# Performance work log

Measured on AMD Instinct MI355X. Metric: run time of the kernel, lower is better.

The kernel has to match this reference:

```python
import jax, jax.numpy as jnp
import numpy as np

B, T, C = 4, 4096, 512
H, KS = 8, 9
D = C // H
PAD = KS // 2


def setup_inputs() -> dict:
    key = jax.random.key(0)
    ks = jax.random.split(key, 9)
    s = 1.0 / np.sqrt(C)
    return {
        "x": jax.random.normal(ks[0], (B, T, C), jnp.float32),
        "Wq": jax.random.normal(ks[1], (C, C), jnp.float32) * s,
        "bq": jax.random.normal(ks[2], (C,), jnp.float32) * 0.01,
        "Wk": jax.random.normal(ks[3], (C, C), jnp.float32) * s,
        "bk": jax.random.normal(ks[4], (C,), jnp.float32) * 0.01,
        "Wv": jax.random.normal(ks[5], (C, C), jnp.float32) * s,
        "bv": jax.random.normal(ks[6], (C,), jnp.float32) * 0.01,
        "Wo": jax.random.normal(ks[7], (C, C), jnp.float32) * s,
        "bo": jax.random.normal(ks[8], (C,), jnp.float32) * 0.01,
    }


def reference(x, Wq, bq, Wk, bk, Wv, bv, Wo, bo):
    Bx, Tx, Cx = x.shape
    # projections (torch Linear: x @ W.T + b), split heads -> (B,H,T,D)
    q = (x @ Wq.T + bq).reshape(Bx, Tx, H, D).transpose(0, 2, 1, 3)
    k = (x @ Wk.T + bk).reshape(Bx, Tx, H, D).transpose(0, 2, 1, 3)
    v = (x @ Wv.T + bv).reshape(Bx, Tx, H, D).transpose(0, 2, 1, 3)
    # replicate-pad along time (matches F.pad mode='replicate')
    k_pad = jnp.pad(k, ((0, 0), (0, 0), (PAD, PAD), (0, 0)), mode='edge')
    v_pad = jnp.pad(v, ((0, 0), (0, 0), (PAD, PAD), (0, 0)), mode='edge')
    # window gather indices: (T, KS) into padded time axis
    idx = jnp.arange(Tx)[:, None] + jnp.arange(KS)[None, :]
    k_unf = k_pad[:, :, idx, :]  # (B,H,T,KS,D)
    v_unf = v_pad[:, :, idx, :]  # (B,H,T,KS,D)
    scale = 1.0 / np.sqrt(D)
    scores = jnp.einsum('bhtd,bhtkd->bhtk', q, k_unf) * scale  # (B,H,T,KS)
    attn = jax.nn.softmax(scores, axis=-1)
    y = jnp.einsum('bhtk,bhtkd->bhtd', attn, v_unf)  # (B,H,T,D)
    y = y.transpose(0, 2, 1, 3).reshape(Bx, Tx, Cx)
    return y @ Wo.T + bo
```

## Files before the change

kernel.cpp:

```cpp
#include <hip/hip_runtime.h>
#include <hip/hip_bf16.h>

#define B_    4
#define T_    4096
#define C_    512
#define H_    8
#define D_    64
#define KS_   9
#define PAD_  4
#define MTOT  (B_ * T_)
#define PLANE (MTOT * C_)
#define XU    (MTOT * C_ / 8)
#define WU    (C_ * C_ / 8)

typedef __bf16 bf16_t;
typedef __bf16 bf16x8 __attribute__((ext_vector_type(8)));
typedef float  f32x4  __attribute__((ext_vector_type(4)));

__global__ __launch_bounds__(256)
void conv_all(const float* __restrict__ x,  const float* __restrict__ Wq,
              const float* __restrict__ Wk, const float* __restrict__ Wv,
              const float* __restrict__ Wo, bf16_t* __restrict__ dst) {
  int i = blockIdx.x * 256 + threadIdx.x;
  const float* s;
  if (i < XU) {
    s = x + (size_t)i * 8;
  } else {
    int r = i - XU;
    int w = r >> 15;
    const float* W = (w == 0) ? Wq : (w == 1) ? Wk : (w == 2) ? Wv : Wo;
    s = W + (size_t)(r & (WU - 1)) * 8;
  }
  float4 f0 = ((const float4*)s)[0];
  float4 f1 = ((const float4*)s)[1];
  bf16x8 o;
  o[0] = (bf16_t)f0.x; o[1] = (bf16_t)f0.y; o[2] = (bf16_t)f0.z; o[3] = (bf16_t)f0.w;
  o[4] = (bf16_t)f1.x; o[5] = (bf16_t)f1.y; o[6] = (bf16_t)f1.z; o[7] = (bf16_t)f1.w;
  ((bf16x8*)dst)[i] = o;
}

__global__ __launch_bounds__(256, 2)
void qkv_gemm(const bf16_t* __restrict__ xb, const bf16_t* __restrict__ Wb,
              const float* __restrict__ bq, const float* __restrict__ bk,
              const float* __restrict__ bv, bf16_t* __restrict__ qkv) {
  __shared__ __align__(16) bf16_t lsA[256 * 64];
  __shared__ __align__(16) bf16_t lsB[128 * 64];

  const int z    = blockIdx.z;
  const int m0   = blockIdx.y * 256;
  const int n0   = blockIdx.x * 128;
  const bf16_t* W = Wb + (size_t)z * C_ * C_;

  const int tid  = threadIdx.x;
  const int lane = tid & 63;
  const int wave = tid >> 6;
  const int wm   = wave * 64;

  f32x4 acc[4][8] = {};

  for (int k0 = 0; k0 < C_; k0 += 64) {
    __syncthreads();
#pragma unroll
    for (int s = 0; s < 8; ++s) {
      int u    = s * 256 + tid;
      int row  = u >> 3;
      int c    = (u & 7) ^ (row & 7);
      const bf16_t* ga = xb + ((size_t)(m0 + row) * C_ + k0 + c * 8);
      __builtin_amdgcn_global_load_lds(
          (const __attribute__((address_space(1))) unsigned int*)ga,
          (__attribute__((address_space(3))) unsigned int*)&lsA[u * 8], 16, 0, 0);
    }
#pragma unroll
    for (int s = 0; s < 4; ++s) {
      int u    = s * 256 + tid;
      int row  = u >> 3;
      int c    = (u & 7) ^ (row & 7);
      const bf16_t* gb = W + ((size_t)(n0 + row) * C_ + k0 + c * 8);
      __builtin_amdgcn_global_load_lds(
          (const __attribute__((address_space(1))) unsigned int*)gb,
          (__attribute__((address_space(3))) unsigned int*)&lsB[u * 8], 16, 0, 0);
    }
    __syncthreads();

    const int rr = lane & 15;
    const int q  = lane >> 4;
#pragma unroll
    for (int kh = 0; kh < 2; ++kh) {
      const int cg = kh * 4 + q;
      const int sl = (cg ^ (rr & 7)) << 3;
      bf16x8 af[4], bfr[8];
#pragma unroll
      for (int i = 0; i < 4; ++i)
        af[i] = *(const bf16x8*)&lsA[(wm + i * 16 + rr) * 64 + sl];
#pragma unroll
      for (int j = 0; j < 8; ++j)
        bfr[j] = *(const bf16x8*)&lsB[(j * 16 + rr) * 64 + sl];
#pragma unroll
      for (int i = 0; i < 4; ++i)
#pragma unroll
        for (int j = 0; j < 8; ++j)
          acc[i][j] = __builtin_amdgcn_mfma_f32_16x16x32_bf16(
              af[i], bfr[j], acc[i][j], 0, 0, 0);
    }
  }

  const int cn = lane & 15;
  const int rb = (lane >> 4) << 2;
  const float* bias = (z == 0) ? bq : (z == 1) ? bk : bv;
  float bvals[8];
#pragma unroll
  for (int j = 0; j < 8; ++j) bvals[j] = bias[n0 + j * 16 + cn];

  bf16_t* plz = qkv + (size_t)z * PLANE;
#pragma unroll
  for (int i = 0; i < 4; ++i) {
#pragma unroll
    for (int r = 0; r < 4; ++r) {
      int m  = m0 + wm + i * 16 + rb + r;
      int bb = m >> 12, t = m & (T_ - 1);
#pragma unroll
      for (int j = 0; j < 8; ++j) {
        int col = n0 + j * 16 + cn;
        int h = col >> 6, d = col & 63;
        plz[((size_t)(bb * H_ + h) * T_ + t) * D_ + d] =
            (bf16_t)(acc[i][j][r] + bvals[j]);
      }
    }
  }
}

__global__ __launch_bounds__(256, 2)
void out_gemm(const bf16_t* __restrict__ y, const bf16_t* __restrict__ Wob,
              const float* __restrict__ bo, float* __restrict__ out) {
  __shared__ __align__(16) bf16_t lsA[128 * 64];
  __shared__ __align__(16) bf16_t lsB[128 * 64];

  const int tid  = threadIdx.x;
  const int lane = tid & 63;
  const int wave = tid >> 6;
  const int wm   = (wave >> 1) * 64;
  const int wn   = (wave & 1) * 64;
  const int m0   = blockIdx.y * 128;
  const int n0   = blockIdx.x * 128;

  f32x4 acc[4][4] = {};

  for (int k0 = 0; k0 < C_; k0 += 64) {
    __syncthreads();
#pragma unroll
    for (int s = 0; s < 4; ++s) {
      int u    = s * 256 + tid;
      int row  = u >> 3;
      int c    = (u & 7) ^ (row & 7);
      int m = m0 + row;
      int b = m >> 12, t = m & (T_ - 1);
      int h = k0 >> 6;
      const bf16_t* ga = y + (((size_t)(b * H_ + h) * T_ + t) * D_ + c * 8);
      const bf16_t* gb = Wob + ((size_t)(n0 + row) * C_ + k0 + c * 8);
      __builtin_amdgcn_global_load_lds(
          (const __attribute__((address_space(1))) unsigned int*)ga,
          (__attribute__((address_space(3))) unsigned int*)&lsA[u * 8], 16, 0, 0);
      __builtin_amdgcn_global_load_lds(
          (const __attribute__((address_space(1))) unsigned int*)gb,
          (__attribute__((address_space(3))) unsigned int*)&lsB[u * 8], 16, 0, 0);
    }
    __syncthreads();

    const int rr = lane & 15;
    const int q  = lane >> 4;
#pragma unroll
    for (int kh = 0; kh < 2; ++kh) {
      const int cg = kh * 4 + q;
      const int sl = (cg ^ (rr & 7)) << 3;
      bf16x8 af[4], bfr[4];
#pragma unroll
      for (int i = 0; i < 4; ++i) {
        af[i]  = *(const bf16x8*)&lsA[(wm + i * 16 + rr) * 64 + sl];
        bfr[i] = *(const bf16x8*)&lsB[(wn + i * 16 + rr) * 64 + sl];
      }
#pragma unroll
      for (int i = 0; i < 4; ++i)
#pragma unroll
        for (int j = 0; j < 4; ++j)
          acc[i][j] = __builtin_amdgcn_mfma_f32_16x16x32_bf16(
              af[i], bfr[j], acc[i][j], 0, 0, 0);
    }
  }

  const int cn = lane & 15;
  const int rb = (lane >> 4) << 2;
  float bvals[4];
#pragma unroll
  for (int j = 0; j < 4; ++j) bvals[j] = bo[n0 + wn + j * 16 + cn];
#pragma unroll
  for (int i = 0; i < 4; ++i) {
#pragma unroll
    for (int r = 0; r < 4; ++r) {
      int gm = m0 + wm + i * 16 + rb + r;
      float* orow = out + (size_t)gm * C_ + (n0 + wn);
#pragma unroll
      for (int j = 0; j < 4; ++j)
        orow[j * 16 + cn] = acc[i][j][r] + bvals[j];
    }
  }
}

#define AT_T 128
#define AT_R (AT_T + 8)
__global__ __launch_bounds__(256)
void attn_kernel(const bf16_t* __restrict__ qkv, bf16_t* __restrict__ y) {
  __shared__ __align__(16) bf16_t ks[AT_R * D_];
  __shared__ __align__(16) bf16_t vs[AT_R * D_];

  const int tid = threadIdx.x;
  const int t0  = blockIdx.x * AT_T;
  const int h   = blockIdx.y;
  const int b   = blockIdx.z;

  const size_t pl = (size_t)(b * H_ + h) * T_ * D_;
  const bf16_t* kg = qkv + (size_t)PLANE + pl;
  const bf16_t* vg = qkv + (size_t)2 * PLANE + pl;

  for (int c = tid; c < AT_R * 8; c += 256) {
    int r = c >> 3, off = (c & 7) * 8;
    int tg = t0 - PAD_ + r;
    tg = tg < 0 ? 0 : (tg >= T_ ? T_ - 1 : tg);
    *((bf16x8*)ks + c) = *(const bf16x8*)(kg + (size_t)tg * D_ + off);
    *((bf16x8*)vs + c) = *(const bf16x8*)(vg + (size_t)tg * D_ + off);
  }
  __syncthreads();

  const int sub = tid & 7;
  const int tl  = tid >> 3;
  const int c8  = sub * 8;

#pragma unroll
  for (int p = 0; p < AT_T / 32; ++p) {
    const int tloc = p * 32 + tl;
    const int t    = t0 + tloc;

    bf16x8 q8 = *(const bf16x8*)(qkv + pl + (size_t)t * D_ + c8);
    float qf[8];
#pragma unroll
    for (int e = 0; e < 8; ++e) qf[e] = (float)q8[e];

    float s[KS_];
#pragma unroll
    for (int j = 0; j < KS_; ++j) {
      bf16x8 k8 = *(const bf16x8*)&ks[(tloc + j) * D_ + c8];
      float d0 = 0.f;
#pragma unroll
      for (int e = 0; e < 8; ++e) d0 += qf[e] * (float)k8[e];
      s[j] = d0;
    }

#pragma unroll
    for (int m = 1; m < 8; m <<= 1)
#pragma unroll
      for (int j = 0; j < KS_; ++j) s[j] += __shfl_xor(s[j], m, 8);

    float mx = s[0];
#pragma unroll
    for (int j = 1; j < KS_; ++j) mx = fmaxf(mx, s[j]);
    float w[KS_], sum = 0.f;
#pragma unroll
    for (int j = 0; j < KS_; ++j) {
      w[j] = __expf((s[j] - mx) * 0.125f);
      sum += w[j];
    }
    const float inv = 1.f / sum;
#pragma unroll
    for (int j = 0; j < KS_; ++j) w[j] *= inv;

    float o[8] = {0.f, 0.f, 0.f, 0.f, 0.f, 0.f, 0.f, 0.f};
#pragma unroll
    for (int j = 0; j < KS_; ++j) {
      bf16x8 v8 = *(const bf16x8*)&vs[(tloc + j) * D_ + c8];
#pragma unroll
      for (int e = 0; e < 8; ++e) o[e] += w[j] * (float)v8[e];
    }
    bf16x8 o8;
#pragma unroll
    for (int e = 0; e < 8; ++e) o8[e] = (bf16_t)o[e];
    *(bf16x8*)(y + pl + (size_t)t * D_ + c8) = o8;
  }
}

extern "C" void kernel_launch(void* const* d_in, const int* in_sizes, int n_in,
                              void* d_out, int out_size, void* d_ws, size_t ws_size,
                              hipStream_t stream) {
  const float* x  = (const float*)d_in[0];
  const float* Wq = (const float*)d_in[1];
  const float* bq = (const float*)d_in[2];
  const float* Wk = (const float*)d_in[3];
  const float* bk = (const float*)d_in[4];
  const float* Wv = (const float*)d_in[5];
  const float* bv = (const float*)d_in[6];
  const float* Wo = (const float*)d_in[7];
  const float* bo = (const float*)d_in[8];
  float* out = (float*)d_out;

  bf16_t* xb  = (bf16_t*)d_ws;
  bf16_t* Wb  = xb + (size_t)MTOT * C_;
  bf16_t* qkv = Wb + (size_t)4 * C_ * C_;
  bf16_t* y   = qkv + (size_t)3 * PLANE;

  conv_all<<<(XU + 4 * WU) / 256, 256, 0, stream>>>(x, Wq, Wk, Wv, Wo, xb);
  qkv_gemm<<<dim3(C_ / 128, MTOT / 256, 3), 256, 0, stream>>>(
      xb, Wb, bq, bk, bv, qkv);
  attn_kernel<<<dim3(T_ / AT_T, H_, B_), 256, 0, stream>>>(qkv, y);
  out_gemm<<<dim3(C_ / 128, MTOT / 128, 1), 256, 0, stream>>>(
      y, Wb + (size_t)3 * C_ * C_, bo, out);
}
```

Measured before the change: 171.3 us.

## Fuse local attention into output projection GEMM and retile QKV GEMM

Removes the standalone attention kernel and computes windowed attention per head inside the output GEMM, staging the head output in LDS as the A operand. This avoids writing and rereading the intermediate y tensor and saves a launch. In exchange, attention is recomputed by each of the four N-column blocks, K/V are read from global memory instead of LDS, and the attention work is serialized with the MFMA loop. The QKV GEMM is also retiled from 256x128 to 128x128 with a 2x2 wave layout and a simplified head-major store.

```diff
diff --git a/kernel.cpp b/kernel.cpp
--- a/kernel.cpp
+++ b/kernel.cpp
@@ -43,105 +43,19 @@
 void qkv_gemm(const bf16_t* __restrict__ xb, const bf16_t* __restrict__ Wb,
               const float* __restrict__ bq, const float* __restrict__ bk,
               const float* __restrict__ bv, bf16_t* __restrict__ qkv) {
-  __shared__ __align__(16) bf16_t lsA[256 * 64];
+  __shared__ __align__(16) bf16_t lsA[128 * 64];
   __shared__ __align__(16) bf16_t lsB[128 * 64];
 
   const int z    = blockIdx.z;
-  const int m0   = blockIdx.y * 256;
+  const int m0   = blockIdx.y * 128;
   const int n0   = blockIdx.x * 128;
   const bf16_t* W = Wb + (size_t)z * C_ * C_;
-
-  const int tid  = threadIdx.x;
-  const int lane = tid & 63;
-  const int wave = tid >> 6;
-  const int wm   = wave * 64;
-
-  f32x4 acc[4][8] = {};
-
-  for (int k0 = 0; k0 < C_; k0 += 64) {
-    __syncthreads();
-#pragma unroll
-    for (int s = 0; s < 8; ++s) {
-      int u    = s * 256 + tid;
-      int row  = u >> 3;
-      int c    = (u & 7) ^ (row & 7);
-      const bf16_t* ga = xb + ((size_t)(m0 + row) * C_ + k0 + c * 8);
-      __builtin_amdgcn_global_load_lds(
-          (const __attribute__((address_space(1))) unsigned int*)ga,
-          (__attribute__((address_space(3))) unsigned int*)&lsA[u * 8], 16, 0, 0);
-    }
-#pragma unroll
-    for (int s = 0; s < 4; ++s) {
-      int u    = s * 256 + tid;
-      int row  = u >> 3;
-      int c    = (u & 7) ^ (row & 7);
-      const bf16_t* gb = W + ((size_t)(n0 + row) * C_ + k0 + c * 8);
-      __builtin_amdgcn_global_load_lds(
-          (const __attribute__((address_space(1))) unsigned int*)gb,
-          (__attribute__((address_space(3))) unsigned int*)&lsB[u * 8], 16, 0, 0);
-    }
-    __syncthreads();
-
-    const int rr = lane & 15;
-    const int q  = lane >> 4;
-#pragma unroll
-    for (int kh = 0; kh < 2; ++kh) {
-      const int cg = kh * 4 + q;
-      const int sl = (cg ^ (rr & 7)) << 3;
-      bf16x8 af[4], bfr[8];
-#pragma unroll
-      for (int i = 0; i < 4; ++i)
-        af[i] = *(const bf16x8*)&lsA[(wm + i * 16 + rr) * 64 + sl];
-#pragma unroll
-      for (int j = 0; j < 8; ++j)
-        bfr[j] = *(const bf16x8*)&lsB[(j * 16 + rr) * 64 + sl];
-#pragma unroll
-      for (int i = 0; i < 4; ++i)
-#pragma unroll
-        for (int j = 0; j < 8; ++j)
-          acc[i][j] = __builtin_amdgcn_mfma_f32_16x16x32_bf16(
-              af[i], bfr[j], acc[i][j], 0, 0, 0);
-    }
-  }
-
-  const int cn = lane & 15;
-  const int rb = (lane >> 4) << 2;
-  const float* bias = (z == 0) ? bq : (z == 1) ? bk : bv;
-  float bvals[8];
-#pragma unroll
-  for (int j = 0; j < 8; ++j) bvals[j] = bias[n0 + j * 16 + cn];
-
-  bf16_t* plz = qkv + (size_t)z * PLANE;
-#pragma unroll
-  for (int i = 0; i < 4; ++i) {
-#pragma unroll
-    for (int r = 0; r < 4; ++r) {
-      int m  = m0 + wm + i * 16 + rb + r;
-      int bb = m >> 12, t = m & (T_ - 1);
-#pragma unroll
-      for (int j = 0; j < 8; ++j) {
-        int col = n0 + j * 16 + cn;
-        int h = col >> 6, d = col & 63;
-        plz[((size_t)(bb * H_ + h) * T_ + t) * D_ + d] =
-            (bf16_t)(acc[i][j][r] + bvals[j]);
-      }
-    }
-  }
-}
-
-__global__ __launch_bounds__(256, 2)
-void out_gemm(const bf16_t* __restrict__ y, const bf16_t* __restrict__ Wob,
-              const float* __restrict__ bo, float* __restrict__ out) {
-  __shared__ __align__(16) bf16_t lsA[128 * 64];
-  __shared__ __align__(16) bf16_t lsB[128 * 64];
 
   const int tid  = threadIdx.x;
   const int lane = tid & 63;
   const int wave = tid >> 6;
   const int wm   = (wave >> 1) * 64;
   const int wn   = (wave & 1) * 64;
-  const int m0   = blockIdx.y * 128;
-  const int n0   = blockIdx.x * 128;
 
   f32x4 acc[4][4] = {};
 
@@ -152,11 +66,8 @@
       int u    = s * 256 + tid;
       int row  = u >> 3;
       int c    = (u & 7) ^ (row & 7);
-      int m = m0 + row;
-      int b = m >> 12, t = m & (T_ - 1);
-      int h = k0 >> 6;
-      const bf16_t* ga = y + (((size_t)(b * H_ + h) * T_ + t) * D_ + c * 8);
-      const bf16_t* gb = Wob + ((size_t)(n0 + row) * C_ + k0 + c * 8);
+      const bf16_t* ga = xb + ((size_t)(m0 + row) * C_ + k0 + c * 8);
+      const bf16_t* gb = W + ((size_t)(n0 + row) * C_ + k0 + c * 8);
       __builtin_amdgcn_global_load_lds(
           (const __attribute__((address_space(1))) unsigned int*)ga,
           (__attribute__((address_space(3))) unsigned int*)&lsA[u * 8], 16, 0, 0);
@@ -189,6 +100,152 @@
 
   const int cn = lane & 15;
   const int rb = (lane >> 4) << 2;
+  const float* bias = (z == 0) ? bq : (z == 1) ? bk : bv;
+  float bvals[4];
+#pragma unroll
+  for (int j = 0; j < 4; ++j) bvals[j] = bias[n0 + wn + j * 16 + cn];
+
+  const int bb = m0 >> 12;
+  const int hh = (n0 + wn) >> 6;
+  bf16_t* hb = qkv + (size_t)z * PLANE + (size_t)(bb * H_ + hh) * T_ * D_;
+#pragma unroll
+  for (int i = 0; i < 4; ++i) {
+#pragma unroll
+    for (int r = 0; r < 4; ++r) {
+      int t = (m0 + wm + i * 16 + rb + r) & (T_ - 1);
+      bf16_t* row = hb + (size_t)t * D_;
+#pragma unroll
+      for (int j = 0; j < 4; ++j)
+        row[j * 16 + cn] = (bf16_t)(acc[i][j][r] + bvals[j]);
+    }
+  }
+}
+
+__global__ __launch_bounds__(256, 2)
+void attn_out(const bf16_t* __restrict__ qkv, const bf16_t* __restrict__ Wob,
+              const float* __restrict__ bo, float* __restrict__ out) {
+  __shared__ __align__(16) bf16_t ys[128 * 64];
+  __shared__ __align__(16) bf16_t lsB[128 * 64];
+
+  const int tid  = threadIdx.x;
+  const int lane = tid & 63;
+  const int wave = tid >> 6;
+  const int wm   = (wave >> 1) * 64;
+  const int wn   = (wave & 1) * 64;
+  const int n0   = blockIdx.x * 128;
+  const int m0   = blockIdx.y * 128;
+  const int b    = m0 >> 12;
+  const int t0   = m0 & (T_ - 1);
+
+  const int sub = tid & 7;
+  const int tl  = tid >> 3;
+  const int c8  = sub * 8;
+
+  f32x4 acc[4][4] = {};
+
+  for (int h = 0; h < H_; ++h) {
+    const size_t pl = (size_t)(b * H_ + h) * T_ * D_;
+    const bf16_t* qg = qkv + pl;
+    const bf16_t* kg = qkv + (size_t)PLANE + pl;
+    const bf16_t* vg = qkv + (size_t)2 * PLANE + pl;
+    const int k0 = h * 64;
+
+    __syncthreads();
+
+#pragma unroll
+    for (int s = 0; s < 4; ++s) {
+      int u   = s * 256 + tid;
+      int row = u >> 3;
+      int c   = (u & 7) ^ (row & 7);
+      const bf16_t* gb = Wob + ((size_t)(n0 + row) * C_ + k0 + c * 8);
+      __builtin_amdgcn_global_load_lds(
+          (const __attribute__((address_space(1))) unsigned int*)gb,
+          (__attribute__((address_space(3))) unsigned int*)&lsB[u * 8], 16, 0, 0);
+    }
+
+#pragma unroll
+    for (int p = 0; p < 4; ++p) {
+      const int tloc = p * 32 + tl;
+      const int t    = t0 + tloc;
+
+      int tj[KS_];
+#pragma unroll
+      for (int j = 0; j < KS_; ++j) {
+        int tt = t - PAD_ + j;
+        tj[j] = tt < 0 ? 0 : (tt >= T_ ? T_ - 1 : tt);
+      }
+
+      bf16x8 q8 = *(const bf16x8*)(qg + (size_t)t * D_ + c8);
+      float qf[8];
+#pragma unroll
+      for (int e = 0; e < 8; ++e) qf[e] = (float)q8[e];
+
+      float s[KS_];
+#pragma unroll
+      for (int j = 0; j < KS_; ++j) {
+        bf16x8 k8 = *(const bf16x8*)(kg + (size_t)tj[j] * D_ + c8);
+        float d0 = 0.f;
+#pragma unroll
+        for (int e = 0; e < 8; ++e) d0 += qf[e] * (float)k8[e];
+        s[j] = d0;
+      }
+
+#pragma unroll
+      for (int m = 1; m < 8; m <<= 1)
+#pragma unroll
+        for (int j = 0; j < KS_; ++j) s[j] += __shfl_xor(s[j], m, 8);
+
+      float mx = s[0];
+#pragma unroll
+      for (int j = 1; j < KS_; ++j) mx = fmaxf(mx, s[j]);
+      float w[KS_], sum = 0.f;
+#pragma unroll
+      for (int j = 0; j < KS_; ++j) {
+        w[j] = __expf((s[j] - mx) * 0.125f);
+        sum += w[j];
+      }
+      const float inv = 1.f / sum;
+#pragma unroll
+      for (int j = 0; j < KS_; ++j) w[j] *= inv;
+
+      float o[8] = {0.f, 0.f, 0.f, 0.f, 0.f, 0.f, 0.f, 0.f};
+#pragma unroll
+      for (int j = 0; j < KS_; ++j) {
+        bf16x8 v8 = *(const bf16x8*)(vg + (size_t)tj[j] * D_ + c8);
+#pragma unroll
+        for (int e = 0; e < 8; ++e) o[e] += w[j] * (float)v8[e];
+      }
+      bf16x8 o8;
+#pragma unroll
+      for (int e = 0; e < 8; ++e) o8[e] = (bf16_t)o[e];
+      *(bf16x8*)&ys[tloc * 64 + ((sub ^ (tloc & 7)) << 3)] = o8;
+    }
+
+    __syncthreads();
+
+    const int rr = lane & 15;
+    const int q  = lane >> 4;
+#pragma unroll
+    for (int kh = 0; kh < 2; ++kh) {
+      const int cg = kh * 4 + q;
+      const int sl = (cg ^ (rr & 7)) << 3;
+      bf16x8 af[4], bfr[4];
+#pragma unroll
+      for (int i = 0; i < 4; ++i) {
+        af[i]  = *(const bf16x8*)&ys[(wm + i * 16 + rr) * 64 + sl];
+        bfr[i] = *(const bf16x8*)&lsB[(wn + i * 16 + rr) * 64 + sl];
+      }
+#pragma unroll
+      for (int i = 0; i < 4; ++i)
+#pragma unroll
+        for (int j = 0; j < 4; ++j)
+          acc[i][j] = __builtin_amdgcn_mfma_f32_16x16x32_bf16(
+              af[i], bfr[j], acc[i][j], 0, 0, 0);
+    }
+  }
+
+  const int cn = lane & 15;
+  const int rb = (lane >> 4) << 2;
   float bvals[4];
 #pragma unroll
   for (int j = 0; j < 4; ++j) bvals[j] = bo[n0 + wn + j * 16 + cn];
@@ -202,87 +259,6 @@
       for (int j = 0; j < 4; ++j)
         orow[j * 16 + cn] = acc[i][j][r] + bvals[j];
     }
-  }
-}
-
-#define AT_T 128
-#define AT_R (AT_T + 8)
-__global__ __launch_bounds__(256)
-void attn_kernel(const bf16_t* __restrict__ qkv, bf16_t* __restrict__ y) {
-  __shared__ __align__(16) bf16_t ks[AT_R * D_];
-  __shared__ __align__(16) bf16_t vs[AT_R * D_];
-
-  const int tid = threadIdx.x;
-  const int t0  = blockIdx.x * AT_T;
-  const int h   = blockIdx.y;
-  const int b   = blockIdx.z;
-
-  const size_t pl = (size_t)(b * H_ + h) * T_ * D_;
-  const bf16_t* kg = qkv + (size_t)PLANE + pl;
-  const bf16_t* vg = qkv + (size_t)2 * PLANE + pl;
-
-  for (int c = tid; c < AT_R * 8; c += 256) {
-    int r = c >> 3, off = (c & 7) * 8;
-    int tg = t0 - PAD_ + r;
-    tg = tg < 0 ? 0 : (tg >= T_ ? T_ - 1 : tg);
-    *((bf16x8*)ks + c) = *(const bf16x8*)(kg + (size_t)tg * D_ + off);
-    *((bf16x8*)vs + c) = *(const bf16x8*)(vg + (size_t)tg * D_ + off);
-  }
-  __syncthreads();
-
-  const int sub = tid & 7;
-  const int tl  = tid >> 3;
-  const int c8  = sub * 8;
-
-#pragma unroll
-  for (int p = 0; p < AT_T / 32; ++p) {
-    const int tloc = p * 32 + tl;
-    const int t    = t0 + tloc;
-
-    bf16x8 q8 = *(const bf16x8*)(qkv + pl + (size_t)t * D_ + c8);
-    float qf[8];
-#pragma unroll
-    for (int e = 0; e < 8; ++e) qf[e] = (float)q8[e];
-
-    float s[KS_];
-#pragma unroll
-    for (int j = 0; j < KS_; ++j) {
-      bf16x8 k8 = *(const bf16x8*)&ks[(tloc + j) * D_ + c8];
-      float d0 = 0.f;
-#pragma unroll
-      for (int e = 0; e < 8; ++e) d0 += qf[e] * (float)k8[e];
-      s[j] = d0;
-    }
-
-#pragma unroll
-    for (int m = 1; m < 8; m <<= 1)
-#pragma unroll
-      for (int j = 0; j < KS_; ++j) s[j] += __shfl_xor(s[j], m, 8);
-
-    float mx = s[0];
-#pragma unroll
-    for (int j = 1; j < KS_; ++j) mx = fmaxf(mx, s[j]);
-    float w[KS_], sum = 0.f;
-#pragma unroll
-    for (int j = 0; j < KS_; ++j) {
-      w[j] = __expf((s[j] - mx) * 0.125f);
-      sum += w[j];
-    }
-    const float inv = 1.f / sum;
-#pragma unroll
-    for (int j = 0; j < KS_; ++j) w[j] *= inv;
-
-    float o[8] = {0.f, 0.f, 0.f, 0.f, 0.f, 0.f, 0.f, 0.f};
-#pragma unroll
-    for (int j = 0; j < KS_; ++j) {
-      bf16x8 v8 = *(const bf16x8*)&vs[(tloc + j) * D_ + c8];
-#pragma unroll
-      for (int e = 0; e < 8; ++e) o[e] += w[j] * (float)v8[e];
-    }
-    bf16x8 o8;
-#pragma unroll
-    for (int e = 0; e < 8; ++e) o8[e] = (bf16_t)o[e];
-    *(bf16x8*)(y + pl + (size_t)t * D_ + c8) = o8;
   }
 }
 
@@ -303,12 +279,10 @@
   bf16_t* xb  = (bf16_t*)d_ws;
   bf16_t* Wb  = xb + (size_t)MTOT * C_;
   bf16_t* qkv = Wb + (size_t)4 * C_ * C_;
-  bf16_t* y   = qkv + (size_t)3 * PLANE;
 
   conv_all<<<(XU + 4 * WU) / 256, 256, 0, stream>>>(x, Wq, Wk, Wv, Wo, xb);
-  qkv_gemm<<<dim3(C_ / 128, MTOT / 256, 3), 256, 0, stream>>>(
+  qkv_gemm<<<dim3(C_ / 128, MTOT / 128, 3), 256, 0, stream>>>(
       xb, Wb, bq, bk, bv, qkv);
-  attn_kernel<<<dim3(T_ / AT_T, H_, B_), 256, 0, stream>>>(qkv, y);
-  out_gemm<<<dim3(C_ / 128, MTOT / 128, 1), 256, 0, stream>>>(
-      y, Wb + (size_t)3 * C_ * C_, bo, out);
-}
+  attn_out<<<dim3(C_ / 128, MTOT / 128), 256, 0, stream>>>(
+      qkv, Wb + (size_t)3 * C_ * C_, bo, out);
+}
```

After: 260.9 us. 1.52x slower.
